# Optimization experiments

Hardware: AMD Instinct MI355X
Metric: run time of the kernel (lower is better)

## Reference

```python
import jax, jax.numpy as jnp
import numpy as np

N, L, C, KF = 32, 1024, 3, 256
H = C * KF            # hidden_dim = 768
M = 3072              # mlp_dim
EPS = 1e-6


def setup_inputs() -> dict:
    key = jax.random.key(0)
    ks = jax.random.split(key, 14)
    s = lambda fan: 1.0 / np.sqrt(fan)
    return {
        "x": jax.random.normal(ks[0], (N, L, H), dtype=jnp.float32),
        # per-channel QKV linears: Linear(k_factor, 3*k_factor) for each channel
        "W_qkv": jax.random.normal(ks[1], (C, KF, 3 * KF), dtype=jnp.float32) * s(KF),
        "b_qkv": jax.random.normal(ks[2], (C, 3 * KF), dtype=jnp.float32) * 0.01,
        "W_out": jax.random.normal(ks[3], (KF, KF), dtype=jnp.float32) * s(KF),
        "b_out": jax.random.normal(ks[4], (KF,), dtype=jnp.float32) * 0.01,
        "ln1_g": jnp.ones((H,), jnp.float32),
        "ln1_b": jnp.zeros((H,), jnp.float32),
        "ln2_g": jnp.ones((H,), jnp.float32),
        "ln2_b": jnp.zeros((H,), jnp.float32),
        "W1": jax.random.normal(ks[5], (H, M), dtype=jnp.float32) * s(H),
        "b1": jax.random.normal(ks[6], (M,), dtype=jnp.float32) * 1e-6,
        "W2": jax.random.normal(ks[7], (M, H), dtype=jnp.float32) * s(M),
        "b2": jax.random.normal(ks[8], (H,), dtype=jnp.float32) * 1e-6,
    }


def _ln(x, g, b):
    mu = jnp.mean(x, axis=-1, keepdims=True)
    var = jnp.mean(jnp.square(x - mu), axis=-1, keepdims=True)
    return (x - mu) * jax.lax.rsqrt(var + EPS) * g + b


def _criss_cross_attn(h, W_qkv, b_qkv, W_out, b_out):
    # h: [N, L, H]; hidden layout is channel-major: (C, KF)
    hc = h.reshape(h.shape[0], h.shape[1], C, KF)
    qkv = jnp.einsum("nlck,ckd->nlcd", hc, W_qkv) + b_qkv      # [N,L,C,3KF]
    q, k, v = jnp.split(qkv, 3, axis=-1)                        # each [N,L,C,KF]
    # move k_factor axis before channel axis: [N,L,KF,C]
    q = jnp.swapaxes(q, -1, -2)
    k = jnp.swapaxes(k, -1, -2)
    v = jnp.swapaxes(v, -1, -2)
    # outer-product scores over channels: [N,L,KF,C,C]
    scores = q[..., :, None] * k[..., None, :] / np.sqrt(KF)
    attn = jax.nn.softmax(scores, axis=-1)
    # einsum 'ijklm,ijkl->ijkm': sum over first channel axis
    ctx = jnp.einsum("nlkcd,nlkc->nlkd", attn, v)               # [N,L,KF,C]
    ctx = jnp.swapaxes(ctx, -1, -2)                             # [N,L,C,KF]
    out = ctx @ W_out + b_out                                   # fc_out per k_factor
    return out.reshape(h.shape[0], h.shape[1], H)


def reference(x, W_qkv, b_qkv, W_out, b_out, ln1_g, ln1_b, ln2_g, ln2_b, W1, b1, W2, b2):
    h = _ln(x, ln1_g, ln1_b)
    a = _criss_cross_attn(h, W_qkv, b_qkv, W_out, b_out)
    xr = a + x                                                   # residual (dropout=0)
    y = _ln(xr, ln2_g, ln2_b)
    y = jax.nn.gelu(y @ W1 + b1, approximate=False) @ W2 + b2    # MLPBlock
    return xr + y
```

## Files before the change

kernel.cpp:

```cpp
#include <hip/hip_runtime.h>
#include <hip/hip_bf16.h>
#include <math.h>

typedef __attribute__((ext_vector_type(8))) short short8;
typedef __attribute__((ext_vector_type(4))) float f32x4;

__device__ __forceinline__ float bf2f(__hip_bfloat16 h) { return __bfloat162float(h); }
__device__ __forceinline__ __hip_bfloat16 f2bf(float f) { return __float2bfloat16(f); }

__device__ __forceinline__ float gelu_f(float v) {
  const float u = v * (0.7978845608f + 0.0356774081f * v * v);
  const float e = __expf(2.0f * u);
  const float t = 1.0f - 2.0f * __builtin_amdgcn_rcpf(e + 1.0f);
  return 0.5f * v * (1.0f + t);
}

__global__ __launch_bounds__(256) void ln_kernel(
    const float* __restrict__ in, const float* __restrict__ g,
    const float* __restrict__ b, __hip_bfloat16* __restrict__ out)
{
  __shared__ float sm1[4], sm2[4];
  const int row = blockIdx.x;
  const int tid = threadIdx.x;
  const float* p = in + (size_t)row * 768;
  float x0 = p[tid], x1 = p[tid + 256], x2 = p[tid + 512];
  float s = x0 + x1 + x2;
  #pragma unroll
  for (int off = 32; off > 0; off >>= 1) s += __shfl_down(s, off, 64);
  const int l = tid & 63, w = tid >> 6;
  if (l == 0) sm1[w] = s;
  __syncthreads();
  const float mu = (sm1[0] + sm1[1] + sm1[2] + sm1[3]) * (1.0f / 768.0f);
  const float d0 = x0 - mu, d1 = x1 - mu, d2 = x2 - mu;
  float ss = d0*d0 + d1*d1 + d2*d2;
  #pragma unroll
  for (int off = 32; off > 0; off >>= 1) ss += __shfl_down(ss, off, 64);
  if (l == 0) sm2[w] = ss;
  __syncthreads();
  const float var = (sm2[0] + sm2[1] + sm2[2] + sm2[3]) * (1.0f / 768.0f);
  const float rstd = rsqrtf(var + 1e-6f);
  __hip_bfloat16* q = out + (size_t)row * 768;
  q[tid]       = f2bf(d0 * rstd * g[tid]       + b[tid]);
  q[tid + 256] = f2bf(d1 * rstd * g[tid + 256] + b[tid + 256]);
  q[tid + 512] = f2bf(d2 * rstd * g[tid + 512] + b[tid + 512]);
}

__global__ __launch_bounds__(256) void attn_kernel(
    const __hip_bfloat162* __restrict__ qkv, __hip_bfloat162* __restrict__ ctx)
{
  const long t = (long)blockIdx.x * 256 + threadIdx.x;
  const long row = t >> 7;
  const int kp = (int)(t & 127);
  const __hip_bfloat162* p = qkv + row * 1152;
  float q[3][2], k[3][2], v[3][2];
  #pragma unroll
  for (int c = 0; c < 3; ++c) {
    __hip_bfloat162 qq = p[c*384 + kp];
    __hip_bfloat162 kk = p[c*384 + 128 + kp];
    __hip_bfloat162 vv = p[c*384 + 256 + kp];
    q[c][0] = __low2float(qq); q[c][1] = __high2float(qq);
    k[c][0] = __low2float(kk); k[c][1] = __high2float(kk);
    v[c][0] = __low2float(vv); v[c][1] = __high2float(vv);
  }
  float o[3][2] = {};
  #pragma unroll
  for (int u = 0; u < 2; ++u) {
    #pragma unroll
    for (int c = 0; c < 3; ++c) {
      const float s0 = q[c][u]*k[0][u]*0.0625f, s1 = q[c][u]*k[1][u]*0.0625f, s2 = q[c][u]*k[2][u]*0.0625f;
      const float m = fmaxf(s0, fmaxf(s1, s2));
      const float e0 = __expf(s0-m), e1 = __expf(s1-m), e2 = __expf(s2-m);
      const float inv = v[c][u] / (e0 + e1 + e2);
      o[0][u] += e0*inv; o[1][u] += e1*inv; o[2][u] += e2*inv;
    }
  }
  __hip_bfloat162* po = ctx + row * 384;
  #pragma unroll
  for (int d = 0; d < 3; ++d)
    po[d*128 + kp] = __hip_bfloat162{f2bf(o[d][0]), f2bf(o[d][1])};
}

__global__ __launch_bounds__(256) void transpose_bf16_kernel(
    const float* __restrict__ in, __hip_bfloat16* __restrict__ out, int K, int N)
{
  __shared__ float tile[32][33];
  in  += (size_t)blockIdx.z * K * N;
  out += (size_t)blockIdx.z * K * N;
  const int n0 = blockIdx.x * 32;
  const int k0 = blockIdx.y * 32;
  const int tx = threadIdx.x & 31, ty = threadIdx.x >> 5;
  #pragma unroll
  for (int r = 0; r < 32; r += 8)
    tile[ty + r][tx] = in[(size_t)(k0 + ty + r) * N + n0 + tx];
  __syncthreads();
  #pragma unroll
  for (int r = 0; r < 32; r += 8)
    out[(size_t)(n0 + ty + r) * K + k0 + tx] = f2bf(tile[tx][ty + r]);
}

#define BM 128
#define BN 128
#define BK 32

template<int MODE>
__global__ __launch_bounds__(256) void gemm_bt_kernel(
    const __hip_bfloat16* __restrict__ A, int lda, long strideA,
    const __hip_bfloat16* __restrict__ Bt, int ldb, long strideB,
    float* __restrict__ Cf, __hip_bfloat16* __restrict__ Cb, int ldc, long strideC,
    const float* __restrict__ bias, long strideBias,
    const float* __restrict__ res,
    int K)
{
  __shared__ __align__(16) char sAll[2 * 16384];

  const int z = blockIdx.z;
  A    += (size_t)z * strideA;
  Bt   += (size_t)z * strideB;
  bias += (size_t)z * strideBias;
  const long cOff = (long)z * strideC;

  const long tileM = (long)blockIdx.x * BM;
  const int  tileN = blockIdx.y * BN;

  const int tid  = threadIdx.x;
  const int lane = tid & 63;
  const int wv   = tid >> 6;
  const int waveM = (wv & 1) * 64;
  const int waveN = (wv >> 1) * 64;

  const int srow  = tid >> 2;
  const int selem = ((tid & 3) ^ ((srow >> 1) & 3)) * 8;
  const int frow = lane & 15;
  const int fkb  = (((lane >> 4) ^ ((frow >> 1) & 3)) << 4);

  const __hip_bfloat16* Ab = A  + tileM * (size_t)lda + selem;
  const __hip_bfloat16* Bb = Bt + (long)tileN * (size_t)ldb + selem;

  f32x4 acc[4][4] = {};

  const int T = K / BK;

  {
    #pragma unroll
    for (int hh = 0; hh < 2; ++hh) {
      const int r = hh * 64 + srow;
      __builtin_amdgcn_global_load_lds(
          (const __attribute__((address_space(1))) void*)(Ab + (size_t)r * lda),
          (__attribute__((address_space(3))) void*)(sAll + hh*4096 + tid*16), 16, 0, 0);
      __builtin_amdgcn_global_load_lds(
          (const __attribute__((address_space(1))) void*)(Bb + (size_t)r * ldb),
          (__attribute__((address_space(3))) void*)(sAll + 8192 + hh*4096 + tid*16), 16, 0, 0);
    }
  }

  for (int t = 0; t < T; ++t) {
    const int buf = (t & 1) * 16384;
    if (t + 1 < T) {
      const int nbuf = 16384 - buf;
      const int k0 = (t + 1) * BK;
      #pragma unroll
      for (int hh = 0; hh < 2; ++hh) {
        const int r = hh * 64 + srow;
        __builtin_amdgcn_global_load_lds(
            (const __attribute__((address_space(1))) void*)(Ab + (size_t)r * lda + k0),
            (__attribute__((address_space(3))) void*)(sAll + nbuf + hh*4096 + tid*16), 16, 0, 0);
        __builtin_amdgcn_global_load_lds(
            (const __attribute__((address_space(1))) void*)(Bb + (size_t)r * ldb + k0),
            (__attribute__((address_space(3))) void*)(sAll + nbuf + 8192 + hh*4096 + tid*16), 16, 0, 0);
      }
      asm volatile("s_waitcnt vmcnt(4)" ::: "memory");
    } else {
      asm volatile("s_waitcnt vmcnt(0)" ::: "memory");
    }
    __builtin_amdgcn_s_barrier();

    const char* sAb = sAll + buf;
    const char* sBb = sAb + 8192;
    short8 aF[4], bF[4];
    #pragma unroll
    for (int i = 0; i < 4; ++i)
      aF[i] = *(const short8*)(sAb + (waveM + i*16 + frow) * 64 + fkb);
    #pragma unroll
    for (int j = 0; j < 4; ++j)
      bF[j] = *(const short8*)(sBb + (waveN + j*16 + frow) * 64 + fkb);
    #pragma unroll
    for (int i = 0; i < 4; ++i)
      #pragma unroll
      for (int j = 0; j < 4; ++j)
        acc[i][j] = __builtin_amdgcn_mfma_f32_16x16x32_bf16(aF[i], bF[j], acc[i][j], 0, 0, 0);

    __builtin_amdgcn_s_barrier();
  }

  #pragma unroll
  for (int i = 0; i < 4; ++i) {
    const long row0 = tileM + waveM + i*16 + ((lane >> 4) * 4);
    #pragma unroll
    for (int j = 0; j < 4; ++j) {
      const int col = tileN + waveN + j*16 + (lane & 15);
      const float bv = bias[col];
      #pragma unroll
      for (int r = 0; r < 4; ++r) {
        const long idx = cOff + (row0 + r) * (long)ldc + col;
        const float v = acc[i][j][r] + bv;
        if (MODE == 0) {
          Cb[idx] = f2bf(v);
        } else if (MODE == 1 || MODE == 3) {
          Cf[idx] = v + res[idx];
        } else {
          Cb[idx] = f2bf(gelu_f(v));
        }
      }
    }
  }
}

#define GLL16(src, dst) __builtin_amdgcn_global_load_lds( \
    (const __attribute__((address_space(1))) void*)(src), \
    (__attribute__((address_space(3))) void*)(dst), 16, 0, 0)

#define STAGE_A(h, bufo, koff) do { \
    GLL16(Ab + (size_t)((h)*128 + 0) * lda + (koff), sAll + (bufo) + (h)*16384 + 0*8192 + tid*16); \
    GLL16(Ab + (size_t)((h)*128 + 64) * lda + (koff), sAll + (bufo) + (h)*16384 + 1*8192 + tid*16); \
  } while (0)
#define STAGE_B(h, bufo, koff) do { \
    GLL16(Bb + (size_t)((h)*128 + 0) * ldb + (koff), sAll + (bufo) + 32768 + (h)*16384 + 0*8192 + tid*16); \
    GLL16(Bb + (size_t)((h)*128 + 64) * ldb + (koff), sAll + (bufo) + 32768 + (h)*16384 + 1*8192 + tid*16); \
  } while (0)

template<int MODE>
__global__ __launch_bounds__(512, 2) void gemm256_kernel(
    const __hip_bfloat16* __restrict__ A, int lda, long strideA,
    const __hip_bfloat16* __restrict__ Bt, int ldb, long strideB,
    float* __restrict__ Cf, __hip_bfloat16* __restrict__ Cb, int ldc, long strideC,
    const float* __restrict__ bias, long strideBias,
    const float* __restrict__ res,
    int K)
{
  __shared__ __align__(16) char sAll[2 * 65536];

  const int z = blockIdx.z;
  A    += (size_t)z * strideA;
  Bt   += (size_t)z * strideB;
  bias += (size_t)z * strideBias;
  const long cOff = (long)z * strideC;

  const long tileM = (long)blockIdx.x * 256;
  const int  tileN = blockIdx.y * 256;

  const int tid  = threadIdx.x;
  const int lane = tid & 63;
  const int wv   = tid >> 6;
  const int wm   = wv & 1;
  const int wn   = wv >> 1;

  const int srow  = tid >> 3;
  const int selem = ((tid & 7) ^ (srow & 7)) * 8;

  const __hip_bfloat16* Ab = A  + (tileM + srow) * (size_t)lda + selem;
  const __hip_bfloat16* Bb = Bt + ((long)tileN + srow) * (size_t)ldb + selem;

  const int fk   = lane >> 4;
  const int fx   = lane & 7;
  const int arow = (wm*64 + (lane & 15)) * 128;
  const int brow = (wn*32 + (lane & 15)) * 128;
  const int ax0  = ((0*4 + fk) ^ fx) * 16;
  const int ax1  = ((1*4 + fk) ^ fx) * 16;

  f32x4 acc[2][2][4][2] = {};
  const int T = K / 64;

  STAGE_A(0, 0, 0);
  STAGE_B(0, 0, 0);
  STAGE_B(1, 0, 0);
  STAGE_A(1, 0, 0);

  for (int t = 0; t < T; ++t) {
    const int buf  = (t & 1) * 65536;
    const int nbuf = 65536 - buf;
    const int kn   = ((t + 1 < T) ? (t + 1) : t) * 64;

    short8 aF[4][2], bF0[2][2], bF1[2][2];

    asm volatile("s_waitcnt vmcnt(4)" ::: "memory");
    __builtin_amdgcn_s_barrier();
    STAGE_A(0, nbuf, kn);
    {
      const char* sA = sAll + buf;
      const char* sB = sAll + buf + 32768;
      #pragma unroll
      for (int i = 0; i < 4; ++i) {
        aF[i][0] = *(const short8*)(sA + arow + i*2048 + ax0);
        aF[i][1] = *(const short8*)(sA + arow + i*2048 + ax1);
      }
      #pragma unroll
      for (int j = 0; j < 2; ++j) {
        bF0[j][0] = *(const short8*)(sB + brow + j*2048 + ax0);
        bF0[j][1] = *(const short8*)(sB + brow + j*2048 + ax1);
      }
    }
    __builtin_amdgcn_s_setprio(1);
    #pragma unroll
    for (int i = 0; i < 4; ++i)
      #pragma unroll
      for (int j = 0; j < 2; ++j) {
        acc[0][0][i][j] = __builtin_amdgcn_mfma_f32_16x16x32_bf16(aF[i][0], bF0[j][0], acc[0][0][i][j], 0, 0, 0);
        acc[0][0][i][j] = __builtin_amdgcn_mfma_f32_16x16x32_bf16(aF[i][1], bF0[j][1], acc[0][0][i][j], 0, 0, 0);
      }
    __builtin_amdgcn_s_setprio(0);

    STAGE_B(0, nbuf, kn);
    asm volatile("s_waitcnt vmcnt(6)" ::: "memory");
    __builtin_amdgcn_s_barrier();
    {
      const char* sB = sAll + buf + 32768 + 16384;
      #pragma unroll
      for (int j = 0; j < 2; ++j) {
        bF1[j][0] = *(const short8*)(sB + brow + j*2048 + ax0);
        bF1[j][1] = *(const short8*)(sB + brow + j*2048 + ax1);
      }
    }
    __builtin_amdgcn_s_setprio(1);
    #pragma unroll
    for (int i = 0; i < 4; ++i)
      #pragma unroll
      for (int j = 0; j < 2; ++j) {
        acc[0][1][i][j] = __builtin_amdgcn_mfma_f32_16x16x32_bf16(aF[i][0], bF1[j][0], acc[0][1][i][j], 0, 0, 0);
        acc[0][1][i][j] = __builtin_amdgcn_mfma_f32_16x16x32_bf16(aF[i][1], bF1[j][1], acc[0][1][i][j], 0, 0, 0);
      }
    __builtin_amdgcn_s_setprio(0);

    STAGE_B(1, nbuf, kn);
    asm volatile("s_waitcnt vmcnt(6)" ::: "memory");
    __builtin_amdgcn_s_barrier();
    {
      const char* sA = sAll + buf + 16384;
      #pragma unroll
      for (int i = 0; i < 4; ++i) {
        aF[i][0] = *(const short8*)(sA + arow + i*2048 + ax0);
        aF[i][1] = *(const short8*)(sA + arow + i*2048 + ax1);
      }
    }
    __builtin_amdgcn_s_setprio(1);
    #pragma unroll
    for (int i = 0; i < 4; ++i)
      #pragma unroll
      for (int j = 0; j < 2; ++j) {
        acc[1][1][i][j] = __builtin_amdgcn_mfma_f32_16x16x32_bf16(aF[i][0], bF1[j][0], acc[1][1][i][j], 0, 0, 0);
        acc[1][1][i][j] = __builtin_amdgcn_mfma_f32_16x16x32_bf16(aF[i][1], bF1[j][1], acc[1][1][i][j], 0, 0, 0);
      }
    __builtin_amdgcn_s_setprio(0);

    STAGE_A(1, nbuf, kn);
    __builtin_amdgcn_s_setprio(1);
    #pragma unroll
    for (int i = 0; i < 4; ++i)
      #pragma unroll
      for (int j = 0; j < 2; ++j) {
        acc[1][0][i][j] = __builtin_amdgcn_mfma_f32_16x16x32_bf16(aF[i][0], bF0[j][0], acc[1][0][i][j], 0, 0, 0);
        acc[1][0][i][j] = __builtin_amdgcn_mfma_f32_16x16x32_bf16(aF[i][1], bF0[j][1], acc[1][0][i][j], 0, 0, 0);
      }
    __builtin_amdgcn_s_setprio(0);
  }

  asm volatile("s_waitcnt vmcnt(0)" ::: "memory");

  #pragma unroll
  for (int ih = 0; ih < 2; ++ih)
    #pragma unroll
    for (int jh = 0; jh < 2; ++jh)
      #pragma unroll
      for (int i = 0; i < 4; ++i) {
        const long row0 = tileM + ih*128 + wm*64 + i*16 + ((lane >> 4) * 4);
        #pragma unroll
        for (int j = 0; j < 2; ++j) {
          const int col = tileN + jh*128 + wn*32 + j*16 + (lane & 15);
          const float bv = bias[col];
          #pragma unroll
          for (int r = 0; r < 4; ++r) {
            const long idx = cOff + (row0 + r) * (long)ldc + col;
            const float v = acc[ih][jh][i][j][r] + bv;
            if (MODE == 0) {
              Cb[idx] = f2bf(v);
            } else if (MODE == 1 || MODE == 3) {
              Cf[idx] = v + res[idx];
            } else {
              Cb[idx] = f2bf(gelu_f(v));
            }
          }
        }
      }
}

extern "C" void kernel_launch(void* const* d_in, const int* in_sizes, int n_in,
                              void* d_out, int out_size, void* d_ws, size_t ws_size,
                              hipStream_t stream)
{
  const float* x     = (const float*)d_in[0];
  const float* W_qkv = (const float*)d_in[1];
  const float* b_qkv = (const float*)d_in[2];
  const float* W_out = (const float*)d_in[3];
  const float* b_out = (const float*)d_in[4];
  const float* ln1_g = (const float*)d_in[5];
  const float* ln1_b = (const float*)d_in[6];
  const float* ln2_g = (const float*)d_in[7];
  const float* ln2_b = (const float*)d_in[8];
  const float* W1    = (const float*)d_in[9];
  const float* b1    = (const float*)d_in[10];
  const float* W2    = (const float*)d_in[11];
  const float* b2    = (const float*)d_in[12];
  float* out = (float*)d_out;

  char* ws = (char*)d_ws;
  __hip_bfloat16* h     = (__hip_bfloat16*)(ws + 0);
  __hip_bfloat16* qkv   = (__hip_bfloat16*)(ws + 50331648);
  __hip_bfloat16* ctx   = (__hip_bfloat16*)(ws + 0);
  __hip_bfloat16* act   = (__hip_bfloat16*)(ws + 0);
  __hip_bfloat16* yln   = (__hip_bfloat16*)(ws + 201326592);
  __hip_bfloat16* wqkvT = (__hip_bfloat16*)(ws + 251658240);
  __hip_bfloat16* woutT = (__hip_bfloat16*)(ws + 252837888);
  __hip_bfloat16* w1T   = (__hip_bfloat16*)(ws + 252968960);
  __hip_bfloat16* w2T   = (__hip_bfloat16*)(ws + 257687552);

  transpose_bf16_kernel<<<dim3(768/32, 256/32, 3), 256, 0, stream>>>(W_qkv, wqkvT, 256, 768);
  transpose_bf16_kernel<<<dim3(256/32, 256/32, 1), 256, 0, stream>>>(W_out, woutT, 256, 256);
  transpose_bf16_kernel<<<dim3(3072/32, 768/32, 1), 256, 0, stream>>>(W1, w1T, 768, 3072);
  transpose_bf16_kernel<<<dim3(768/32, 3072/32, 1), 256, 0, stream>>>(W2, w2T, 3072, 768);

  ln_kernel<<<32768, 256, 0, stream>>>(x, ln1_g, ln1_b, h);

  gemm256_kernel<0><<<dim3(32768/256, 768/256, 3), 512, 0, stream>>>(
      h, 768, 256, wqkvT, 256, 768*256, nullptr, qkv, 2304, 768, b_qkv, 768, nullptr, 256);

  attn_kernel<<<16384, 256, 0, stream>>>((const __hip_bfloat162*)qkv, (__hip_bfloat162*)ctx);

  gemm_bt_kernel<1><<<dim3(98304/BM, 256/BN, 1), 256, 0, stream>>>(
      ctx, 256, 0, woutT, 256, 0, out, nullptr, 256, 0, b_out, 0, x, 256);

  ln_kernel<<<32768, 256, 0, stream>>>(out, ln2_g, ln2_b, yln);

  gemm256_kernel<2><<<dim3(32768/256, 3072/256, 1), 512, 0, stream>>>(
      yln, 768, 0, w1T, 768, 0, nullptr, act, 3072, 0, b1, 0, nullptr, 768);

  gemm256_kernel<3><<<dim3(32768/256, 768/256, 1), 512, 0, stream>>>(
      act, 3072, 0, w2T, 3072, 0, out, nullptr, 768, 0, b2, 0, out, 3072);
}
```

Before: 787.2 us.

## Deepen 256-tile GEMM prefetch to stage quarter-tiles two iterations ahead

The 256x256 GEMM loop is restructured so each quarter-tile (A half / B half) is refilled as soon as its LDS region has been read, some of it two k-steps ahead in the same buffer. The old scheme staged the whole next buffer one step ahead. It also adds explicit lgkmcnt waits and sched_barriers so LDS fragment reads finish before the MFMA bursts, and drops the mid-iteration vmcnt waits. This aims to give global loads more latency slack. It relies on the existing barriers to avoid overwriting data other waves still read, and the vmcnt(4) accounting has to stay correct.

```diff
diff --git a/kernel.cpp b/kernel.cpp
--- a/kernel.cpp
+++ b/kernel.cpp
@@ -173,6 +173,7 @@
       asm volatile("s_waitcnt vmcnt(0)" ::: "memory");
     }
     __builtin_amdgcn_s_barrier();
+    asm volatile("" ::: "memory");
 
     const char* sAb = sAll + buf;
     const char* sBb = sAb + 8192;
@@ -219,13 +220,13 @@
     (const __attribute__((address_space(1))) void*)(src), \
     (__attribute__((address_space(3))) void*)(dst), 16, 0, 0)
 
-#define STAGE_A(h, bufo, koff) do { \
-    GLL16(Ab + (size_t)((h)*128 + 0) * lda + (koff), sAll + (bufo) + (h)*16384 + 0*8192 + tid*16); \
-    GLL16(Ab + (size_t)((h)*128 + 64) * lda + (koff), sAll + (bufo) + (h)*16384 + 1*8192 + tid*16); \
+#define STAGE_AH(h, pb, koff) do { \
+    GLL16(Ab + (size_t)((h)*128 + 0 ) * lda + (koff), sAll + (pb)*65536 + (h)*16384 + 0    + tid*16); \
+    GLL16(Ab + (size_t)((h)*128 + 64) * lda + (koff), sAll + (pb)*65536 + (h)*16384 + 8192 + tid*16); \
   } while (0)
-#define STAGE_B(h, bufo, koff) do { \
-    GLL16(Bb + (size_t)((h)*128 + 0) * ldb + (koff), sAll + (bufo) + 32768 + (h)*16384 + 0*8192 + tid*16); \
-    GLL16(Bb + (size_t)((h)*128 + 64) * ldb + (koff), sAll + (bufo) + 32768 + (h)*16384 + 1*8192 + tid*16); \
+#define STAGE_BH(h, pb, koff) do { \
+    GLL16(Bb + (size_t)((h)*128 + 0 ) * ldb + (koff), sAll + (pb)*65536 + 32768 + (h)*16384 + 0    + tid*16); \
+    GLL16(Bb + (size_t)((h)*128 + 64) * ldb + (koff), sAll + (pb)*65536 + 32768 + (h)*16384 + 8192 + tid*16); \
   } while (0)
 
 template<int MODE>
@@ -270,35 +271,42 @@
   f32x4 acc[2][2][4][2] = {};
   const int T = K / 64;
 
-  STAGE_A(0, 0, 0);
-  STAGE_B(0, 0, 0);
-  STAGE_B(1, 0, 0);
-  STAGE_A(1, 0, 0);
+  STAGE_AH(0, 0, 0);
+  STAGE_BH(0, 0, 0);
+  STAGE_BH(1, 0, 0);
+  STAGE_AH(1, 0, 0);
+  {
+    const int k1 = (T > 1 ? 1 : 0) * 64;
+    STAGE_AH(0, 1, k1);
+    STAGE_BH(1, 1, k1);
+  }
 
   for (int t = 0; t < T; ++t) {
-    const int buf  = (t & 1) * 65536;
-    const int nbuf = 65536 - buf;
-    const int kn   = ((t + 1 < T) ? (t + 1) : t) * 64;
+    const int p = t & 1;
+    const int q = p ^ 1;
+    const int kn1 = (t + 1 < T ? t + 1 : T - 1) * 64;
+    const int kn2 = (t + 2 < T ? t + 2 : T - 1) * 64;
+    const char* sA = sAll + p * 65536;
+    const char* sB = sA + 32768;
 
     short8 aF[4][2], bF0[2][2], bF1[2][2];
 
     asm volatile("s_waitcnt vmcnt(4)" ::: "memory");
     __builtin_amdgcn_s_barrier();
-    STAGE_A(0, nbuf, kn);
-    {
-      const char* sA = sAll + buf;
-      const char* sB = sAll + buf + 32768;
-      #pragma unroll
-      for (int i = 0; i < 4; ++i) {
-        aF[i][0] = *(const short8*)(sA + arow + i*2048 + ax0);
-        aF[i][1] = *(const short8*)(sA + arow + i*2048 + ax1);
-      }
-      #pragma unroll
-      for (int j = 0; j < 2; ++j) {
-        bF0[j][0] = *(const short8*)(sB + brow + j*2048 + ax0);
-        bF0[j][1] = *(const short8*)(sB + brow + j*2048 + ax1);
-      }
-    }
+    asm volatile("" ::: "memory");
+    #pragma unroll
+    for (int i = 0; i < 4; ++i) {
+      aF[i][0] = *(const short8*)(sA + arow + i*2048 + ax0);
+      aF[i][1] = *(const short8*)(sA + arow + i*2048 + ax1);
+    }
+    #pragma unroll
+    for (int j = 0; j < 2; ++j) {
+      bF0[j][0] = *(const short8*)(sB + brow + j*2048 + ax0);
+      bF0[j][1] = *(const short8*)(sB + brow + j*2048 + ax1);
+    }
+    STAGE_AH(1, q, kn1);
+    asm volatile("s_waitcnt lgkmcnt(0)" ::: "memory");
+    __builtin_amdgcn_sched_barrier(0);
     __builtin_amdgcn_s_setprio(1);
     #pragma unroll
     for (int i = 0; i < 4; ++i)
@@ -308,18 +316,16 @@
         acc[0][0][i][j] = __builtin_amdgcn_mfma_f32_16x16x32_bf16(aF[i][1], bF0[j][1], acc[0][0][i][j], 0, 0, 0);
       }
     __builtin_amdgcn_s_setprio(0);
-
-    STAGE_B(0, nbuf, kn);
-    asm volatile("s_waitcnt vmcnt(6)" ::: "memory");
     __builtin_amdgcn_s_barrier();
-    {
-      const char* sB = sAll + buf + 32768 + 16384;
-      #pragma unroll
-      for (int j = 0; j < 2; ++j) {
-        bF1[j][0] = *(const short8*)(sB + brow + j*2048 + ax0);
-        bF1[j][1] = *(const short8*)(sB + brow + j*2048 + ax1);
-      }
-    }
+
+    #pragma unroll
+    for (int j = 0; j < 2; ++j) {
+      bF1[j][0] = *(const short8*)(sB + 16384 + brow + j*2048 + ax0);
+      bF1[j][1] = *(const short8*)(sB + 16384 + brow + j*2048 + ax1);
+    }
+    STAGE_BH(0, q, kn1);
+    asm volatile("s_waitcnt lgkmcnt(0)" ::: "memory");
+    __builtin_amdgcn_sched_barrier(0);
     __builtin_amdgcn_s_setprio(1);
     #pragma unroll
     for (int i = 0; i < 4; ++i)
@@ -329,18 +335,16 @@
         acc[0][1][i][j] = __builtin_amdgcn_mfma_f32_16x16x32_bf16(aF[i][1], bF1[j][1], acc[0][1][i][j], 0, 0, 0);
       }
     __builtin_amdgcn_s_setprio(0);
-
-    STAGE_B(1, nbuf, kn);
-    asm volatile("s_waitcnt vmcnt(6)" ::: "memory");
     __builtin_amdgcn_s_barrier();
-    {
-      const char* sA = sAll + buf + 16384;
-      #pragma unroll
-      for (int i = 0; i < 4; ++i) {
-        aF[i][0] = *(const short8*)(sA + arow + i*2048 + ax0);
-        aF[i][1] = *(const short8*)(sA + arow + i*2048 + ax1);
-      }
-    }
+
+    #pragma unroll
+    for (int i = 0; i < 4; ++i) {
+      aF[i][0] = *(const short8*)(sA + 16384 + arow + i*2048 + ax0);
+      aF[i][1] = *(const short8*)(sA + 16384 + arow + i*2048 + ax1);
+    }
+    STAGE_AH(0, p, kn2);
+    asm volatile("s_waitcnt lgkmcnt(0)" ::: "memory");
+    __builtin_amdgcn_sched_barrier(0);
     __builtin_amdgcn_s_setprio(1);
     #pragma unroll
     for (int i = 0; i < 4; ++i)
@@ -351,7 +355,7 @@
       }
     __builtin_amdgcn_s_setprio(0);
 
-    STAGE_A(1, nbuf, kn);
+    STAGE_BH(1, p, kn2);
     __builtin_amdgcn_s_setprio(1);
     #pragma unroll
     for (int i = 0; i < 4; ++i)
```

New measurement: 770.6 us. -2.1%, faster.
